# Kernel tuning notes

Hardware: AMD Instinct MI355X
Metric: run time of the kernel (lower is better)

Reference implementation:

```python
import jax, jax.numpy as jnp
import numpy as np

NUM_CLASSES = 64      # num_classes (centroid_mode='mean': extra_clusters/prototypes unused)
TEMP = 0.1            # contrastive_temp
GLW = 0.5             # global_loss_weight
N, D, B, K = 65536, 512, 4, 16


def setup_inputs() -> dict:
    key = jax.random.key(0)
    k1, k2, k3, k4 = jax.random.split(key, 4)
    S1 = jax.random.normal(k1, (N, D), dtype=jnp.float32)
    S2 = jax.random.normal(k2, (N, D), dtype=jnp.float32)
    seg = jax.random.randint(k3, (N,), 0, NUM_CLASSES)
    # guarantee every class appears, so torch.unique(labels) == arange(NUM_CLASSES)
    seg = seg.at[:NUM_CLASSES].set(jnp.arange(NUM_CLASSES))
    sim = jax.random.uniform(k4, (B, N // B, K), dtype=jnp.float32)
    return {"S1": S1, "S2": S2, "segmentation_map": seg,
            "similarity_matrix": sim}


def reference(S1, S2, segmentation_map, similarity_matrix):
    labels = segmentation_map.reshape(-1)  # [N] int; all classes present
    # --- compute_centroid (mean mode) as one-pass segment reduce ---
    ones = jnp.ones((labels.shape[0],), dtype=S1.dtype)
    counts = jax.ops.segment_sum(ones, labels, num_segments=NUM_CLASSES)      # [C]
    sums = jax.ops.segment_sum(S1, labels, num_segments=NUM_CLASSES)          # [C,D]
    centroids = sums / counts[:, None]                                        # [C,D]
    # --- logits ---
    local_logits = (S1 @ centroids.T) / TEMP    # [N,C]
    global_logits = (S2 @ centroids.T) / TEMP   # [N,C]
    # labels after mask/argmax remap equal the original labels (unique==arange)
    w = similarity_matrix.mean(axis=2).reshape(-1)  # [N]
    def ce(logits):
        logp = jax.nn.log_softmax(logits, axis=-1)
        return -jnp.take_along_axis(logp, labels[:, None], axis=1)[:, 0]
    local_loss = (ce(local_logits) * w).mean()
    global_loss = (ce(global_logits) * w).mean()
    return ((1.0 - GLW) * local_loss + GLW * global_loss) / 2.0
```

## Files before the change

### kernel.cpp

```cpp
#include <hip/hip_runtime.h>

#define NROWS 65536
#define DDIM  512
#define NCLS  64

typedef __attribute__((ext_vector_type(4))) float  floatx4;
typedef __attribute__((ext_vector_type(8))) short  shortx8;
typedef __attribute__((ext_vector_type(4))) short  shortx4;

static constexpr float SCALE = 0.25f / (float)NROWS;

static constexpr size_t OFF_SUMS   = 0;
static constexpr size_t OFF_HIST   = 131072;
static constexpr size_t OFF_CURSOR = 131328;
static constexpr size_t OFF_IDX    = 131584;
static constexpr size_t OFF_CENTBF = 393728;

__device__ __forceinline__ unsigned short f2bf(float f) {
  unsigned u = __float_as_uint(f);
  return (unsigned short)((u + 0x7fffu + ((u >> 16) & 1u)) >> 16);
}

__global__ __launch_bounds__(256) void k_hist(const int* __restrict__ seg,
                                              int* __restrict__ hist) {
  __shared__ int h[NCLS];
  const int t = threadIdx.x;
  if (t < NCLS) h[t] = 0;
  __syncthreads();
  const int4 v = ((const int4*)seg)[blockIdx.x * 256 + t];
  atomicAdd(&h[v.x], 1); atomicAdd(&h[v.y], 1);
  atomicAdd(&h[v.z], 1); atomicAdd(&h[v.w], 1);
  __syncthreads();
  if (t < NCLS) atomicAdd(&hist[t], h[t]);
}

__global__ __launch_bounds__(1024) void k_scatter2(const int* __restrict__ seg,
                                                   const int* __restrict__ hist,
                                                   int* __restrict__ cursor,
                                                   int* __restrict__ idx) {
  __shared__ int lhist[NCLS];
  __shared__ int gbase[NCLS];
  const int t = threadIdx.x;
  if (t < NCLS) lhist[t] = 0;
  __syncthreads();
  const int i0 = blockIdx.x * 2048 + t;
  const int lab0 = seg[i0];
  const int r0 = atomicAdd(&lhist[lab0], 1);
  const int i1 = i0 + 1024;
  const int lab1 = seg[i1];
  const int r1 = atomicAdd(&lhist[lab1], 1);
  __syncthreads();
  if (t < NCLS) {
    const int h = hist[t];
    int x = h;
#pragma unroll
    for (int off = 1; off < 64; off <<= 1) {
      const int y = __shfl_up(x, off, 64);
      if (t >= off) x += y;
    }
    gbase[t] = (x - h) + atomicAdd(&cursor[t], lhist[t]);
  }
  __syncthreads();
  idx[gbase[lab0] + r0] = i0;
  idx[gbase[lab1] + r1] = i1;
}

__global__ __launch_bounds__(256) void k_sumsC(const float* __restrict__ S1,
                                               const int* __restrict__ idx,
                                               const int* __restrict__ hist,
                                               float* __restrict__ sums) {
  __shared__ int sh_start[NCLS + 1];
  __shared__ float red[256];
  const int c  = blockIdx.x >> 3;
  const int qq = blockIdx.x & 7;
  const int t  = threadIdx.x;
  if (t < 64) {
    const int h = hist[t];
    int x = h;
#pragma unroll
    for (int off = 1; off < 64; off <<= 1) {
      const int y = __shfl_up(x, off, 64);
      if (t >= off) x += y;
    }
    sh_start[t] = x - h;
    if (t == 63) sh_start[64] = x;
  }
  __syncthreads();
  const int s0 = sh_start[c];
  const int n  = sh_start[c + 1] - s0;
  const int sub = t >> 6;
  const int col = qq * 64 + (t & 63);
  const int n4 = n >> 2;
  const int base = s0 + sub * n4;
  const int len  = (sub == 3) ? (n - 3 * n4) : n4;
  const float* Sc = S1 + col;
  float a0 = 0.f, a1 = 0.f, a2 = 0.f, a3 = 0.f;
  int j = 0;
  for (; j + 8 <= len; j += 8) {
    const int* ip = idx + base + j;
    const int r0 = ip[0], r1 = ip[1], r2 = ip[2], r3 = ip[3];
    const int r4 = ip[4], r5 = ip[5], r6 = ip[6], r7 = ip[7];
    a0 += Sc[(size_t)r0 * DDIM]; a1 += Sc[(size_t)r1 * DDIM];
    a2 += Sc[(size_t)r2 * DDIM]; a3 += Sc[(size_t)r3 * DDIM];
    a0 += Sc[(size_t)r4 * DDIM]; a1 += Sc[(size_t)r5 * DDIM];
    a2 += Sc[(size_t)r6 * DDIM]; a3 += Sc[(size_t)r7 * DDIM];
  }
  for (; j < len; ++j) a0 += Sc[(size_t)idx[base + j] * DDIM];
  red[t] = a0 + a1 + a2 + a3;
  __syncthreads();
  if (t < 64)
    sums[(size_t)c * DDIM + col] = red[t] + red[t + 64] + red[t + 128] + red[t + 192];
}

__global__ __launch_bounds__(256) void k_cent(const float* __restrict__ sums,
                                              const int* __restrict__ hist,
                                              unsigned short* __restrict__ centbf) {
  const int i = blockIdx.x * 256 + threadIdx.x;
  const int c = i >> 9;
  centbf[i] = f2bf(sums[i] * (10.0f / (float)hist[c]));
}

__global__ __launch_bounds__(256) void k_loss(const float* __restrict__ S1,
                                              const float* __restrict__ S2,
                                              const int* __restrict__ seg,
                                              const float* __restrict__ sim,
                                              const unsigned short* __restrict__ centbf,
                                              float* __restrict__ out) {
  __shared__ __align__(16) char smem[18432];
  short* Sa = (short*)smem;
  short* Cb = (short*)(smem + 9216);
  float* Lg = (float*)smem;

  const int t = threadIdx.x;
  const int g0 = blockIdx.x * 64;
  const bool isS2 = (g0 >= NROWS);
  const float* S = isS2 ? S2 : S1;
  const int i0 = isS2 ? (g0 - NROWS) : g0;

  const int lane = t & 63;
  const int w    = t >> 6;
  const int m    = lane & 15;
  const int quad = lane >> 4;

  floatx4 acc0 = {0.f,0.f,0.f,0.f}, acc1 = {0.f,0.f,0.f,0.f};
  floatx4 acc2 = {0.f,0.f,0.f,0.f}, acc3 = {0.f,0.f,0.f,0.f};

  const int srow = t >> 2;
  const int sfq  = t & 3;

  for (int d0 = 0; d0 < DDIM; d0 += 64) {
    __syncthreads();
    {
      const float* src = &S[(size_t)(i0 + srow) * DDIM + d0];
#pragma unroll
      for (int p = 0; p < 4; ++p) {
        const int col = p * 16 + sfq * 4;
        const float4 v = *(const float4*)&src[col];
        shortx4 b;
        b.x = (short)f2bf(v.x); b.y = (short)f2bf(v.y);
        b.z = (short)f2bf(v.z); b.w = (short)f2bf(v.w);
        *(shortx4*)&Sa[srow * 72 + col] = b;
      }
      const int e0 = sfq * 16;
      const short* cs = (const short*)&centbf[(size_t)srow * DDIM + d0 + e0];
      *(shortx8*)&Cb[srow * 72 + e0]     = *(const shortx8*)cs;
      *(shortx8*)&Cb[srow * 72 + e0 + 8] = *(const shortx8*)(cs + 8);
    }
    __syncthreads();
#pragma unroll
    for (int kk = 0; kk < 64; kk += 32) {
      const shortx8 a = *(const shortx8*)&Sa[(w * 16 + m) * 72 + kk + quad * 8];
      const shortx8 b0 = *(const shortx8*)&Cb[(0  + m) * 72 + kk + quad * 8];
      acc0 = __builtin_amdgcn_mfma_f32_16x16x32_bf16(a, b0, acc0, 0, 0, 0);
      const shortx8 b1 = *(const shortx8*)&Cb[(16 + m) * 72 + kk + quad * 8];
      acc1 = __builtin_amdgcn_mfma_f32_16x16x32_bf16(a, b1, acc1, 0, 0, 0);
      const shortx8 b2 = *(const shortx8*)&Cb[(32 + m) * 72 + kk + quad * 8];
      acc2 = __builtin_amdgcn_mfma_f32_16x16x32_bf16(a, b2, acc2, 0, 0, 0);
      const shortx8 b3 = *(const shortx8*)&Cb[(48 + m) * 72 + kk + quad * 8];
      acc3 = __builtin_amdgcn_mfma_f32_16x16x32_bf16(a, b3, acc3, 0, 0, 0);
    }
  }

  __syncthreads();
#pragma unroll
  for (int r = 0; r < 4; ++r) {
    const int row = w * 16 + quad * 4 + r;
    Lg[row * 68 + 0  + m] = acc0[r];
    Lg[row * 68 + 16 + m] = acc1[r];
    Lg[row * 68 + 32 + m] = acc2[r];
    Lg[row * 68 + 48 + m] = acc3[r];
  }
  __syncthreads();

  if (t < 64) {
    const int r = t;
    float mx = -1e30f;
#pragma unroll
    for (int c4 = 0; c4 < 16; ++c4) {
      const float4 v = *(const float4*)&Lg[r * 68 + c4 * 4];
      mx = fmaxf(mx, fmaxf(fmaxf(v.x, v.y), fmaxf(v.z, v.w)));
    }
    float sum = 0.f;
#pragma unroll
    for (int c4 = 0; c4 < 16; ++c4) {
      const float4 v = *(const float4*)&Lg[r * 68 + c4 * 4];
      sum += __expf(v.x - mx) + __expf(v.y - mx) + __expf(v.z - mx) + __expf(v.w - mx);
    }
    const int lab = seg[i0 + r];
    const float ce = mx + __logf(sum) - Lg[r * 68 + lab];
    const float4* sp = (const float4*)&sim[(size_t)(i0 + r) * 16];
    const float4 w0 = sp[0], w1 = sp[1], w2 = sp[2], w3 = sp[3];
    const float wgt = (w0.x + w0.y + w0.z + w0.w + w1.x + w1.y + w1.z + w1.w +
                       w2.x + w2.y + w2.z + w2.w + w3.x + w3.y + w3.z + w3.w) * (1.0f / 16.0f);
    float v = ce * wgt * SCALE;
#pragma unroll
    for (int off = 32; off > 0; off >>= 1) v += __shfl_down(v, off, 64);
    if (t == 0) atomicAdd(out, v);
  }
}

extern "C" void kernel_launch(void* const* d_in, const int* in_sizes, int n_in,
                              void* d_out, int out_size, void* d_ws, size_t ws_size,
                              hipStream_t stream) {
  const float* S1  = (const float*)d_in[0];
  const float* S2  = (const float*)d_in[1];
  const int*   seg = (const int*)d_in[2];
  const float* sim = (const float*)d_in[3];
  char* ws = (char*)d_ws;
  float* sums   = (float*)(ws + OFF_SUMS);
  int*   hist   = (int*)(ws + OFF_HIST);
  int*   cursor = (int*)(ws + OFF_CURSOR);
  int*   idx    = (int*)(ws + OFF_IDX);
  unsigned short* centbf = (unsigned short*)(ws + OFF_CENTBF);
  float* out = (float*)d_out;

  hipMemsetAsync(ws + OFF_HIST, 0, 512, stream);
  hipMemsetAsync(d_out, 0, sizeof(float), stream);

  k_hist<<<64, 256, 0, stream>>>(seg, hist);
  k_scatter2<<<32, 1024, 0, stream>>>(seg, hist, cursor, idx);
  k_sumsC<<<512, 256, 0, stream>>>(S1, idx, hist, sums);
  k_cent<<<128, 256, 0, stream>>>(sums, hist, centbf);
  k_loss<<<2048, 256, 0, stream>>>(S1, S2, seg, sim, centbf, out);
}
```

Baseline: 335.7 us.

## Fuse centroid normalization into loss kernel with LDS-resident centroids and register-direct A operands

Removes the separate centroid kernel: each loss block normalizes the sums into bf16 centroids and keeps them in a 64 KB swizzled LDS buffer. It then streams S rows directly from global memory into registers as MFMA A operands, prefetching one step ahead, so the per-tile LDS staging and barriers go away. The softmax and cross-entropy now run on the accumulators with 16-lane shuffles instead of an LDS round trip. The gather loop in the sums kernel also prefetches the next eight indices. The cost is that every block redoes the centroid conversion and holds a large LDS allocation, which limits how many blocks fit per CU.

```diff
diff --git a/kernel.cpp b/kernel.cpp
--- a/kernel.cpp
+++ b/kernel.cpp
@@ -6,7 +6,6 @@
 
 typedef __attribute__((ext_vector_type(4))) float  floatx4;
 typedef __attribute__((ext_vector_type(8))) short  shortx8;
-typedef __attribute__((ext_vector_type(4))) short  shortx4;
 
 static constexpr float SCALE = 0.25f / (float)NROWS;
 
@@ -14,7 +13,6 @@
 static constexpr size_t OFF_HIST   = 131072;
 static constexpr size_t OFF_CURSOR = 131328;
 static constexpr size_t OFF_IDX    = 131584;
-static constexpr size_t OFF_CENTBF = 393728;
 
 __device__ __forceinline__ unsigned short f2bf(float f) {
   unsigned u = __float_as_uint(f);
@@ -94,16 +92,29 @@
   const int base = s0 + sub * n4;
   const int len  = (sub == 3) ? (n - 3 * n4) : n4;
   const float* Sc = S1 + col;
+  const int* ip = idx + base;
   float a0 = 0.f, a1 = 0.f, a2 = 0.f, a3 = 0.f;
   int j = 0;
-  for (; j + 8 <= len; j += 8) {
-    const int* ip = idx + base + j;
-    const int r0 = ip[0], r1 = ip[1], r2 = ip[2], r3 = ip[3];
-    const int r4 = ip[4], r5 = ip[5], r6 = ip[6], r7 = ip[7];
-    a0 += Sc[(size_t)r0 * DDIM]; a1 += Sc[(size_t)r1 * DDIM];
-    a2 += Sc[(size_t)r2 * DDIM]; a3 += Sc[(size_t)r3 * DDIM];
-    a0 += Sc[(size_t)r4 * DDIM]; a1 += Sc[(size_t)r5 * DDIM];
-    a2 += Sc[(size_t)r6 * DDIM]; a3 += Sc[(size_t)r7 * DDIM];
+  if (len >= 8) {
+    int r[8];
+#pragma unroll
+    for (int q = 0; q < 8; ++q) r[q] = ip[q];
+    for (; j + 16 <= len; j += 8) {
+      int nr[8];
+#pragma unroll
+      for (int q = 0; q < 8; ++q) nr[q] = ip[j + 8 + q];
+      a0 += Sc[(size_t)r[0] * DDIM]; a1 += Sc[(size_t)r[1] * DDIM];
+      a2 += Sc[(size_t)r[2] * DDIM]; a3 += Sc[(size_t)r[3] * DDIM];
+      a0 += Sc[(size_t)r[4] * DDIM]; a1 += Sc[(size_t)r[5] * DDIM];
+      a2 += Sc[(size_t)r[6] * DDIM]; a3 += Sc[(size_t)r[7] * DDIM];
+#pragma unroll
+      for (int q = 0; q < 8; ++q) r[q] = nr[q];
+    }
+    a0 += Sc[(size_t)r[0] * DDIM]; a1 += Sc[(size_t)r[1] * DDIM];
+    a2 += Sc[(size_t)r[2] * DDIM]; a3 += Sc[(size_t)r[3] * DDIM];
+    a0 += Sc[(size_t)r[4] * DDIM]; a1 += Sc[(size_t)r[5] * DDIM];
+    a2 += Sc[(size_t)r[6] * DDIM]; a3 += Sc[(size_t)r[7] * DDIM];
+    j += 8;
   }
   for (; j < len; ++j) a0 += Sc[(size_t)idx[base + j] * DDIM];
   red[t] = a0 + a1 + a2 + a3;
@@ -112,110 +123,116 @@
     sums[(size_t)c * DDIM + col] = red[t] + red[t + 64] + red[t + 128] + red[t + 192];
 }
 
-__global__ __launch_bounds__(256) void k_cent(const float* __restrict__ sums,
-                                              const int* __restrict__ hist,
-                                              unsigned short* __restrict__ centbf) {
-  const int i = blockIdx.x * 256 + threadIdx.x;
-  const int c = i >> 9;
-  centbf[i] = f2bf(sums[i] * (10.0f / (float)hist[c]));
-}
-
-__global__ __launch_bounds__(256) void k_loss(const float* __restrict__ S1,
-                                              const float* __restrict__ S2,
-                                              const int* __restrict__ seg,
-                                              const float* __restrict__ sim,
-                                              const unsigned short* __restrict__ centbf,
-                                              float* __restrict__ out) {
-  __shared__ __align__(16) char smem[18432];
-  short* Sa = (short*)smem;
-  short* Cb = (short*)(smem + 9216);
-  float* Lg = (float*)smem;
-
+__global__ __launch_bounds__(512, 4) void k_loss(const float* __restrict__ S1,
+                                                 const float* __restrict__ S2,
+                                                 const int* __restrict__ seg,
+                                                 const float* __restrict__ sim,
+                                                 const float* __restrict__ sums,
+                                                 const int* __restrict__ hist,
+                                                 float* __restrict__ out) {
+  __shared__ short cent[NCLS * DDIM];
+  __shared__ float red8[8];
   const int t = threadIdx.x;
-  const int g0 = blockIdx.x * 64;
-  const bool isS2 = (g0 >= NROWS);
+
+  {
+    const int cls = t >> 3;
+    const float inv = 10.0f / (float)hist[cls];
+    const float* sp = sums + (size_t)cls * DDIM;
+#pragma unroll
+    for (int i = 0; i < 8; ++i) {
+      const int g = (t & 7) + i * 8;
+      const float4 x = *(const float4*)(sp + g * 8);
+      const float4 y = *(const float4*)(sp + g * 8 + 4);
+      shortx8 b;
+      b[0] = (short)f2bf(x.x * inv); b[1] = (short)f2bf(x.y * inv);
+      b[2] = (short)f2bf(x.z * inv); b[3] = (short)f2bf(x.w * inv);
+      b[4] = (short)f2bf(y.x * inv); b[5] = (short)f2bf(y.y * inv);
+      b[6] = (short)f2bf(y.z * inv); b[7] = (short)f2bf(y.w * inv);
+      *(shortx8*)&cent[cls * DDIM + ((g ^ (cls & 7)) * 8)] = b;
+    }
+  }
+  __syncthreads();
+
+  const int w    = t >> 6;
+  const int lane = t & 63;
+  const int n    = lane & 15;
+  const int quad = lane >> 4;
+  const int vb   = blockIdx.x * 256;
+  const bool isS2 = (vb >= NROWS);
   const float* S = isS2 ? S2 : S1;
-  const int i0 = isS2 ? (g0 - NROWS) : g0;
-
-  const int lane = t & 63;
-  const int w    = t >> 6;
-  const int m    = lane & 15;
-  const int quad = lane >> 4;
-
-  floatx4 acc0 = {0.f,0.f,0.f,0.f}, acc1 = {0.f,0.f,0.f,0.f};
-  floatx4 acc2 = {0.f,0.f,0.f,0.f}, acc3 = {0.f,0.f,0.f,0.f};
-
-  const int srow = t >> 2;
-  const int sfq  = t & 3;
-
-  for (int d0 = 0; d0 < DDIM; d0 += 64) {
-    __syncthreads();
-    {
-      const float* src = &S[(size_t)(i0 + srow) * DDIM + d0];
-#pragma unroll
-      for (int p = 0; p < 4; ++p) {
-        const int col = p * 16 + sfq * 4;
-        const float4 v = *(const float4*)&src[col];
-        shortx4 b;
-        b.x = (short)f2bf(v.x); b.y = (short)f2bf(v.y);
-        b.z = (short)f2bf(v.z); b.w = (short)f2bf(v.w);
-        *(shortx4*)&Sa[srow * 72 + col] = b;
+  const int i0m = isS2 ? (vb - NROWS) : vb;
+
+  float loss_acc = 0.f;
+#pragma unroll 1
+  for (int s = 0; s < 2; ++s) {
+    const int row0 = i0m + s * 128 + w * 16;
+    const float* Srow = S + (size_t)(row0 + n) * DDIM;
+    floatx4 acc0 = {0,0,0,0}, acc1 = {0,0,0,0}, acc2 = {0,0,0,0}, acc3 = {0,0,0,0};
+    float4 aLo = *(const float4*)(Srow + quad * 8);
+    float4 aHi = *(const float4*)(Srow + quad * 8 + 4);
+#pragma unroll
+    for (int c = 0; c < 16; ++c) {
+      float4 nLo, nHi;
+      if (c < 15) {
+        nLo = *(const float4*)(Srow + (c + 1) * 32 + quad * 8);
+        nHi = *(const float4*)(Srow + (c + 1) * 32 + quad * 8 + 4);
       }
-      const int e0 = sfq * 16;
-      const short* cs = (const short*)&centbf[(size_t)srow * DDIM + d0 + e0];
-      *(shortx8*)&Cb[srow * 72 + e0]     = *(const shortx8*)cs;
-      *(shortx8*)&Cb[srow * 72 + e0 + 8] = *(const shortx8*)(cs + 8);
-    }
-    __syncthreads();
-#pragma unroll
-    for (int kk = 0; kk < 64; kk += 32) {
-      const shortx8 a = *(const shortx8*)&Sa[(w * 16 + m) * 72 + kk + quad * 8];
-      const shortx8 b0 = *(const shortx8*)&Cb[(0  + m) * 72 + kk + quad * 8];
-      acc0 = __builtin_amdgcn_mfma_f32_16x16x32_bf16(a, b0, acc0, 0, 0, 0);
-      const shortx8 b1 = *(const shortx8*)&Cb[(16 + m) * 72 + kk + quad * 8];
-      acc1 = __builtin_amdgcn_mfma_f32_16x16x32_bf16(a, b1, acc1, 0, 0, 0);
-      const shortx8 b2 = *(const shortx8*)&Cb[(32 + m) * 72 + kk + quad * 8];
-      acc2 = __builtin_amdgcn_mfma_f32_16x16x32_bf16(a, b2, acc2, 0, 0, 0);
-      const shortx8 b3 = *(const shortx8*)&Cb[(48 + m) * 72 + kk + quad * 8];
-      acc3 = __builtin_amdgcn_mfma_f32_16x16x32_bf16(a, b3, acc3, 0, 0, 0);
-    }
-  }
-
-  __syncthreads();
-#pragma unroll
-  for (int r = 0; r < 4; ++r) {
-    const int row = w * 16 + quad * 4 + r;
-    Lg[row * 68 + 0  + m] = acc0[r];
-    Lg[row * 68 + 16 + m] = acc1[r];
-    Lg[row * 68 + 32 + m] = acc2[r];
-    Lg[row * 68 + 48 + m] = acc3[r];
-  }
-  __syncthreads();
-
-  if (t < 64) {
-    const int r = t;
-    float mx = -1e30f;
-#pragma unroll
-    for (int c4 = 0; c4 < 16; ++c4) {
-      const float4 v = *(const float4*)&Lg[r * 68 + c4 * 4];
-      mx = fmaxf(mx, fmaxf(fmaxf(v.x, v.y), fmaxf(v.z, v.w)));
-    }
-    float sum = 0.f;
-#pragma unroll
-    for (int c4 = 0; c4 < 16; ++c4) {
-      const float4 v = *(const float4*)&Lg[r * 68 + c4 * 4];
-      sum += __expf(v.x - mx) + __expf(v.y - mx) + __expf(v.z - mx) + __expf(v.w - mx);
-    }
-    const int lab = seg[i0 + r];
-    const float ce = mx + __logf(sum) - Lg[r * 68 + lab];
-    const float4* sp = (const float4*)&sim[(size_t)(i0 + r) * 16];
-    const float4 w0 = sp[0], w1 = sp[1], w2 = sp[2], w3 = sp[3];
-    const float wgt = (w0.x + w0.y + w0.z + w0.w + w1.x + w1.y + w1.z + w1.w +
-                       w2.x + w2.y + w2.z + w2.w + w3.x + w3.y + w3.z + w3.w) * (1.0f / 16.0f);
-    float v = ce * wgt * SCALE;
-#pragma unroll
-    for (int off = 32; off > 0; off >>= 1) v += __shfl_down(v, off, 64);
-    if (t == 0) atomicAdd(out, v);
+      shortx8 af;
+      af[0] = (short)f2bf(aLo.x); af[1] = (short)f2bf(aLo.y);
+      af[2] = (short)f2bf(aLo.z); af[3] = (short)f2bf(aLo.w);
+      af[4] = (short)f2bf(aHi.x); af[5] = (short)f2bf(aHi.y);
+      af[6] = (short)f2bf(aHi.z); af[7] = (short)f2bf(aHi.w);
+      const int gp = ((c * 4 + quad) ^ (n & 7)) * 8;
+      const shortx8 b0 = *(const shortx8*)&cent[(0  + n) * DDIM + gp];
+      acc0 = __builtin_amdgcn_mfma_f32_16x16x32_bf16(af, b0, acc0, 0, 0, 0);
+      const shortx8 b1 = *(const shortx8*)&cent[(16 + n) * DDIM + gp];
+      acc1 = __builtin_amdgcn_mfma_f32_16x16x32_bf16(af, b1, acc1, 0, 0, 0);
+      const shortx8 b2 = *(const shortx8*)&cent[(32 + n) * DDIM + gp];
+      acc2 = __builtin_amdgcn_mfma_f32_16x16x32_bf16(af, b2, acc2, 0, 0, 0);
+      const shortx8 b3 = *(const shortx8*)&cent[(48 + n) * DDIM + gp];
+      acc3 = __builtin_amdgcn_mfma_f32_16x16x32_bf16(af, b3, acc3, 0, 0, 0);
+      aLo = nLo; aHi = nHi;
+    }
+    float ce4[4];
+#pragma unroll
+    for (int r = 0; r < 4; ++r) {
+      float mx = fmaxf(fmaxf(acc0[r], acc1[r]), fmaxf(acc2[r], acc3[r]));
+      mx = fmaxf(mx, __shfl_xor(mx, 1, 16));
+      mx = fmaxf(mx, __shfl_xor(mx, 2, 16));
+      mx = fmaxf(mx, __shfl_xor(mx, 4, 16));
+      mx = fmaxf(mx, __shfl_xor(mx, 8, 16));
+      float se = __expf(acc0[r] - mx) + __expf(acc1[r] - mx) +
+                 __expf(acc2[r] - mx) + __expf(acc3[r] - mx);
+      se += __shfl_xor(se, 1, 16);
+      se += __shfl_xor(se, 2, 16);
+      se += __shfl_xor(se, 4, 16);
+      se += __shfl_xor(se, 8, 16);
+      const int lab = seg[row0 + quad * 4 + r];
+      const int ctl = lab >> 4, nl = lab & 15;
+      float v = (ctl == 0) ? acc0[r] : (ctl == 1) ? acc1[r]
+              : (ctl == 2) ? acc2[r] : acc3[r];
+      const float lv = __shfl(v, nl, 16);
+      ce4[r] = mx + __logf(se) - lv;
+    }
+    if (n < 4) {
+      const int R = row0 + quad * 4 + n;
+      const float4* sp4 = (const float4*)&sim[(size_t)R * 16];
+      const float4 w0 = sp4[0], w1 = sp4[1], w2 = sp4[2], w3 = sp4[3];
+      const float wgt = (w0.x + w0.y + w0.z + w0.w + w1.x + w1.y + w1.z + w1.w +
+                         w2.x + w2.y + w2.z + w2.w + w3.x + w3.y + w3.z + w3.w) * (1.0f / 16.0f);
+      loss_acc += ce4[n] * wgt;
+    }
+  }
+
+  float v = loss_acc * SCALE;
+#pragma unroll
+  for (int off = 1; off < 64; off <<= 1) v += __shfl_xor(v, off, 64);
+  if (lane == 0) red8[w] = v;
+  __syncthreads();
+  if (t == 0) {
+    float sacc = red8[0] + red8[1] + red8[2] + red8[3] +
+                 red8[4] + red8[5] + red8[6] + red8[7];
+    atomicAdd(out, sacc);
   }
 }
 
@@ -231,7 +248,6 @@
   int*   hist   = (int*)(ws + OFF_HIST);
   int*   cursor = (int*)(ws + OFF_CURSOR);
   int*   idx    = (int*)(ws + OFF_IDX);
-  unsigned short* centbf = (unsigned short*)(ws + OFF_CENTBF);
   float* out = (float*)d_out;
 
   hipMemsetAsync(ws + OFF_HIST, 0, 512, stream);
@@ -240,6 +256,5 @@
   k_hist<<<64, 256, 0, stream>>>(seg, hist);
   k_scatter2<<<32, 1024, 0, stream>>>(seg, hist, cursor, idx);
   k_sumsC<<<512, 256, 0, stream>>>(S1, idx, hist, sums);
-  k_cent<<<128, 256, 0, stream>>>(sums, hist, centbf);
-  k_loss<<<2048, 256, 0, stream>>>(S1, S2, seg, sim, centbf, out);
-}
+  k_loss<<<512, 512, 0, stream>>>(S1, S2, seg, sim, sums, hist, out);
+}
```

Measured after the change: 423.7 us. 1.26x slower.
